# Optimization experiments

Hardware: AMD Instinct MI355X
Metric: run time of the kernel (lower is better)

Reference implementation:

```python
import jax, jax.numpy as jnp
import numpy as np

N = 50000      # nodes
E = 800000     # edges
D = 96         # in_dim = out_dim
ED = 17        # edge_dim = RBF_BINS + 1


def setup_inputs() -> dict:
    key = jax.random.key(0)
    ks = jax.random.split(key, 12)
    x = jax.random.normal(ks[0], (N, D), dtype=jnp.float32)
    edge_index = jax.random.randint(ks[1], (2, E), 0, N, dtype=jnp.int64)
    edge_attr = jax.random.uniform(ks[2], (E, ED), dtype=jnp.float32)
    s = 1.0 / np.sqrt(ED)
    W1 = jax.random.uniform(ks[3], (D, ED), jnp.float32, -s, s)
    b1 = jax.random.uniform(ks[4], (D,), jnp.float32, -s, s)
    s = 1.0 / np.sqrt(D)
    W2 = jax.random.uniform(ks[5], (D, D), jnp.float32, -s, s)
    b2 = jax.random.uniform(ks[6], (D,), jnp.float32, -s, s)
    Ws = jax.random.uniform(ks[7], (D, D), jnp.float32, -s, s)
    bs = jax.random.uniform(ks[8], (D,), jnp.float32, -s, s)
    Wn = jax.random.uniform(ks[9], (D, D), jnp.float32, -s, s)
    bn = jax.random.uniform(ks[10], (D,), jnp.float32, -s, s)
    return {"x": x, "edge_index": edge_index, "edge_attr": edge_attr,
            "W1": W1, "b1": b1, "W2": W2, "b2": b2,
            "Ws": Ws, "bs": bs, "Wn": Wn, "bn": bn}


def reference(x, edge_index, edge_attr, W1, b1, W2, b2, Ws, bs, Wn, bn):
    src, dst = edge_index[0], edge_index[1]
    # edge MLP: Linear -> ReLU -> Linear  => per-edge weight [E, D]
    h = jax.nn.relu(edge_attr @ W1.T + b1)
    w = h @ W2.T + b2
    # gather node features at src, weight, scatter-add into dst
    msg = w * x[src]                                   # [E, D]
    agg = jax.ops.segment_sum(msg, dst, num_segments=x.shape[0])  # [N, D]
    return jax.nn.relu(x @ Ws.T + bs + agg @ Wn.T + bn)
```

## Files before the change

kernel.cpp:

```cpp
#include <hip/hip_runtime.h>

#define BLOCK 512
#define TE 64
#define TN 64

typedef float f32x4 __attribute__((ext_vector_type(4)));
typedef short s16x8 __attribute__((ext_vector_type(8)));

static __device__ __forceinline__ unsigned short f2bf(float f) {
    unsigned int u = __float_as_uint(f);
    u += 0x7FFFu + ((u >> 16) & 1u);
    return (unsigned short)(u >> 16);
}
static __device__ __forceinline__ float bf2f(unsigned short s) {
    return __uint_as_float(((unsigned int)s) << 16);
}

__global__ __launch_bounds__(BLOCK, 4) void edge_kernel(
    const float* __restrict__ x,
    const int*   __restrict__ ei,
    const float* __restrict__ ea,
    const float* __restrict__ W1,
    const float* __restrict__ b1,
    const float* __restrict__ W2,
    const float* __restrict__ b2,
    float* __restrict__ agg,
    int N, int E)
{
    __shared__ unsigned short sW2h[96][104];
    __shared__ unsigned short sW2l[96][104];
    __shared__ unsigned short sh_hi[TE][104];
    __shared__ unsigned short sh_lo[TE][104];
    __shared__ float sW1[96][20];
    __shared__ float sea[TE][20];
    __shared__ float sb1[96];
    __shared__ int   ssrc[TE], sdst[TE];

    const int tid  = threadIdx.x;
    const int c    = tid & 31;
    const int g    = tid >> 5;
    const int lane = tid & 63;
    const int wv   = tid >> 6;
    const int mr   = wv & 3;
    const int ng   = wv >> 2;
    const int l15  = lane & 15;
    const int l4   = lane >> 4;

    for (int idx = tid; idx < 96 * 20; idx += BLOCK) {
        int d = idx / 20, k = idx - d * 20;
        sW1[d][k] = (k < 17) ? W1[d * 17 + k] : 0.f;
    }
    for (int idx = tid; idx < 96 * 96; idx += BLOCK) {
        int d = idx / 96, k = idx - d * 96;
        float v = W2[idx];
        unsigned short hb = f2bf(v);
        sW2h[d][k] = hb;
        sW2l[d][k] = f2bf(v - bf2f(hb));
    }
    if (tid < 96) sb1[tid] = b1[tid];

    float bias[3];
    #pragma unroll
    for (int t = 0; t < 3; ++t) bias[t] = b2[(ng * 3 + t) * 16 + l15];

    const int ntiles = (E + TE - 1) / TE;
    for (int tile = blockIdx.x; tile < ntiles; tile += gridDim.x) {
        const int e0 = tile * TE;
        __syncthreads();

        for (int idx = tid; idx < TE * 20; idx += BLOCK) {
            int e = idx / 20, k = idx - e * 20;
            float v = 0.f;
            if (k < 17 && e0 + e < E) v = ea[(size_t)(e0 + e) * 17 + k];
            sea[e][k] = v;
        }
        if (tid < TE) {
            int e = e0 + tid;
            ssrc[tid] = (e < E) ? ei[e] : 0;
            sdst[tid] = (e < E) ? ei[E + e] : 0;
        }
        __syncthreads();

        {
            float hacc[4][3];
            #pragma unroll
            for (int i = 0; i < 4; ++i) {
                hacc[i][0] = sb1[c]; hacc[i][1] = sb1[c + 32]; hacc[i][2] = sb1[c + 64];
            }
            #pragma unroll
            for (int k0 = 0; k0 < 20; k0 += 4) {
                float4 w0 = *(const float4*)&sW1[c][k0];
                float4 w1 = *(const float4*)&sW1[c + 32][k0];
                float4 w2 = *(const float4*)&sW1[c + 64][k0];
                #pragma unroll
                for (int i = 0; i < 4; ++i) {
                    float4 av = *(const float4*)&sea[g * 4 + i][k0];
                    hacc[i][0] = fmaf(av.w, w0.w, fmaf(av.z, w0.z, fmaf(av.y, w0.y, fmaf(av.x, w0.x, hacc[i][0]))));
                    hacc[i][1] = fmaf(av.w, w1.w, fmaf(av.z, w1.z, fmaf(av.y, w1.y, fmaf(av.x, w1.x, hacc[i][1]))));
                    hacc[i][2] = fmaf(av.w, w2.w, fmaf(av.z, w2.z, fmaf(av.y, w2.y, fmaf(av.x, w2.x, hacc[i][2]))));
                }
            }
            #pragma unroll
            for (int i = 0; i < 4; ++i) {
                int e = g * 4 + i;
                #pragma unroll
                for (int j = 0; j < 3; ++j) {
                    int d = c + 32 * j;
                    float v = fmaxf(hacc[i][j], 0.f);
                    unsigned short hb = f2bf(v);
                    sh_hi[e][d] = hb;
                    sh_lo[e][d] = f2bf(v - bf2f(hb));
                }
            }
        }
        __syncthreads();

        f32x4 acc[3];
        #pragma unroll
        for (int t = 0; t < 3; ++t) acc[t] = (f32x4){0.f, 0.f, 0.f, 0.f};

        const int arow = mr * 16 + l15;
        #pragma unroll
        for (int chunk = 0; chunk < 3; ++chunk) {
            const int koff = chunk * 32 + l4 * 8;
            s16x8 a_hi = *(const s16x8*)&sh_hi[arow][koff];
            s16x8 a_lo = *(const s16x8*)&sh_lo[arow][koff];
            #pragma unroll
            for (int t = 0; t < 3; ++t) {
                const int brow = (ng * 3 + t) * 16 + l15;
                s16x8 b_hi = *(const s16x8*)&sW2h[brow][koff];
                s16x8 b_lo = *(const s16x8*)&sW2l[brow][koff];
                acc[t] = __builtin_amdgcn_mfma_f32_16x16x32_bf16(a_hi, b_hi, acc[t], 0, 0, 0);
                acc[t] = __builtin_amdgcn_mfma_f32_16x16x32_bf16(a_hi, b_lo, acc[t], 0, 0, 0);
                acc[t] = __builtin_amdgcn_mfma_f32_16x16x32_bf16(a_lo, b_hi, acc[t], 0, 0, 0);
            }
        }

        #pragma unroll
        for (int t = 0; t < 3; ++t) {
            const int d = (ng * 3 + t) * 16 + l15;
            #pragma unroll
            for (int j = 0; j < 4; ++j) {
                const int el = mr * 16 + l4 * 4 + j;
                const int e  = e0 + el;
                if (e < E) {
                    float wval = acc[t][j] + bias[t];
                    int s = ssrc[el], dn = sdst[el];
                    atomicAdd(&agg[(size_t)dn * 96 + d], wval * x[(size_t)s * 96 + d]);
                }
            }
        }
    }
}

__global__ __launch_bounds__(BLOCK, 4) void node_kernel(
    const float* __restrict__ x,
    const float* __restrict__ agg,
    const float* __restrict__ Ws, const float* __restrict__ bs,
    const float* __restrict__ Wn, const float* __restrict__ bn,
    float* __restrict__ out, int N)
{
    __shared__ float sW[96][100];
    __shared__ float sxa[TN][100];
    __shared__ float sbias[96];

    const int tid = threadIdx.x;
    const int c = tid & 31, g = tid >> 5;
    const int n0 = blockIdx.x * TN;

    if (tid < 96) sbias[tid] = bs[tid] + bn[tid];

    float acc[4][3];
    #pragma unroll
    for (int i = 0; i < 4; ++i)
        for (int j = 0; j < 3; ++j) acc[i][j] = 0.f;

    for (int ph = 0; ph < 2; ++ph) {
        const float* __restrict__ W   = ph ? Wn : Ws;
        const float* __restrict__ src = ph ? agg : x;
        __syncthreads();
        for (int idx = tid; idx < 96 * 24; idx += BLOCK) {
            int d = idx / 24, kq = idx - d * 24;
            *(float4*)&sW[d][kq * 4] = *(const float4*)&W[d * 96 + kq * 4];
        }
        for (int idx = tid; idx < TN * 24; idx += BLOCK) {
            int n = idx / 24, kq = idx - n * 24;
            float4 v = make_float4(0.f, 0.f, 0.f, 0.f);
            if (n0 + n < N) v = *(const float4*)&src[(size_t)(n0 + n) * 96 + kq * 4];
            *(float4*)&sxa[n][kq * 4] = v;
        }
        __syncthreads();
        #pragma unroll 2
        for (int k0 = 0; k0 < 96; k0 += 4) {
            float4 w0 = *(const float4*)&sW[c][k0];
            float4 w1 = *(const float4*)&sW[c + 32][k0];
            float4 w2 = *(const float4*)&sW[c + 64][k0];
            #pragma unroll
            for (int i = 0; i < 4; ++i) {
                float4 xv = *(const float4*)&sxa[g * 4 + i][k0];
                acc[i][0] = fmaf(xv.w, w0.w, fmaf(xv.z, w0.z, fmaf(xv.y, w0.y, fmaf(xv.x, w0.x, acc[i][0]))));
                acc[i][1] = fmaf(xv.w, w1.w, fmaf(xv.z, w1.z, fmaf(xv.y, w1.y, fmaf(xv.x, w1.x, acc[i][1]))));
                acc[i][2] = fmaf(xv.w, w2.w, fmaf(xv.z, w2.z, fmaf(xv.y, w2.y, fmaf(xv.x, w2.x, acc[i][2]))));
            }
        }
    }

    #pragma unroll
    for (int i = 0; i < 4; ++i) {
        int n = n0 + g * 4 + i;
        if (n < N) {
            out[(size_t)n * 96 + c]      = fmaxf(acc[i][0] + sbias[c], 0.f);
            out[(size_t)n * 96 + c + 32] = fmaxf(acc[i][1] + sbias[c + 32], 0.f);
            out[(size_t)n * 96 + c + 64] = fmaxf(acc[i][2] + sbias[c + 64], 0.f);
        }
    }
}

extern "C" void kernel_launch(void* const* d_in, const int* in_sizes, int n_in,
                              void* d_out, int out_size, void* d_ws, size_t ws_size,
                              hipStream_t stream) {
    const float* x  = (const float*)d_in[0];
    const int*   ei = (const int*)d_in[1];
    const float* ea = (const float*)d_in[2];
    const float* W1 = (const float*)d_in[3];
    const float* b1 = (const float*)d_in[4];
    const float* W2 = (const float*)d_in[5];
    const float* b2 = (const float*)d_in[6];
    const float* Ws = (const float*)d_in[7];
    const float* bs = (const float*)d_in[8];
    const float* Wn = (const float*)d_in[9];
    const float* bn = (const float*)d_in[10];
    float* out = (float*)d_out;

    const int N = in_sizes[0] / 96;
    const int E = in_sizes[2] / 17;

    float* agg = (ws_size >= (size_t)N * 96 * sizeof(float)) ? (float*)d_ws : out;
    hipMemsetAsync(agg, 0, (size_t)N * 96 * sizeof(float), stream);

    edge_kernel<<<512, BLOCK, 0, stream>>>(x, ei, ea, W1, b1, W2, b2, agg, N, E);
    node_kernel<<<(N + TN - 1) / TN, BLOCK, 0, stream>>>(x, agg, Ws, bs, Wn, bn, out, N);
}
```

Measured before the change: 342.4 us.

## Software-pipeline edge tiles: prefetch next tile, defer atomics, pre-swizzle MFMA operands

Restructures the edge kernel loop so the next tile's edge attributes and indices are loaded into registers while the current tile computes. The x[src] gathers are issued before the MLP math, and the scatter atomics for the previous tile are deferred into the next iteration. W2 and the hidden activations are stored in LDS in an MFMA-fragment-ordered layout to make the operand loads contiguous and avoid bank conflicts. The goal is to hide global load and atomic latency, at the cost of more registers and possible occupancy loss.

```diff
diff --git a/kernel.cpp b/kernel.cpp
--- a/kernel.cpp
+++ b/kernel.cpp
@@ -3,6 +3,7 @@
 #define BLOCK 512
 #define TE 64
 #define TN 64
+#define NTB 512
 
 typedef float f32x4 __attribute__((ext_vector_type(4)));
 typedef short s16x8 __attribute__((ext_vector_type(8)));
@@ -27,10 +28,10 @@
     float* __restrict__ agg,
     int N, int E)
 {
-    __shared__ unsigned short sW2h[96][104];
-    __shared__ unsigned short sW2l[96][104];
-    __shared__ unsigned short sh_hi[TE][104];
-    __shared__ unsigned short sh_lo[TE][104];
+    __shared__ unsigned short sBh[9216];
+    __shared__ unsigned short sBl[9216];
+    __shared__ unsigned short sAh[3][TE][40];
+    __shared__ unsigned short sAl[3][TE][40];
     __shared__ float sW1[96][20];
     __shared__ float sea[TE][20];
     __shared__ float sb1[96];
@@ -46,6 +47,22 @@
     const int l15  = lane & 15;
     const int l4   = lane >> 4;
 
+    const int ntiles = (E + TE - 1) / TE;
+
+    const int pe = tid >> 3, ps = tid & 7;
+    float pf0 = 0.f, pf1 = 0.f, pf2 = 0.f; int pidx = 0;
+    int tile = blockIdx.x;
+    {
+        int e0n = tile * TE;
+        int ee  = e0n + pe; if (ee >= E) ee = E - 1;
+        const float* er = ea + (size_t)ee * 17;
+        pf0 = er[ps];
+        pf1 = er[ps + 8];
+        if (ps == 0) pf2 = er[16];
+        if (tid < TE)            { int e = e0n + tid;      pidx = (e < E) ? ei[e]     : 0; }
+        else if (tid < 2 * TE)   { int e = e0n + tid - TE; pidx = (e < E) ? ei[E + e] : 0; }
+    }
+
     for (int idx = tid; idx < 96 * 20; idx += BLOCK) {
         int d = idx / 20, k = idx - d * 20;
         sW1[d][k] = (k < 17) ? W1[d * 17 + k] : 0.f;
@@ -54,32 +71,72 @@
         int d = idx / 96, k = idx - d * 96;
         float v = W2[idx];
         unsigned short hb = f2bf(v);
-        sW2h[d][k] = hb;
-        sW2l[d][k] = f2bf(v - bf2f(hb));
+        int ngf = d / 48, tt = (d % 48) / 16, r = d & 15;
+        int ch = k >> 5, kl4 = (k & 31) >> 3, sb = k & 7;
+        int fo = ((((ngf * 3 + tt) * 3 + ch) * 4 + kl4) * 16 + r) * 8 + sb;
+        sBh[fo] = hb;
+        sBl[fo] = f2bf(v - bf2f(hb));
     }
     if (tid < 96) sb1[tid] = b1[tid];
-
-    float bias[3];
+    if (tid < TE) { sea[tid][17] = 0.f; sea[tid][18] = 0.f; sea[tid][19] = 0.f; }
+
+    float bias[3]; int dv[3];
     #pragma unroll
-    for (int t = 0; t < 3; ++t) bias[t] = b2[(ng * 3 + t) * 16 + l15];
-
-    const int ntiles = (E + TE - 1) / TE;
-    for (int tile = blockIdx.x; tile < ntiles; tile += gridDim.x) {
-        const int e0 = tile * TE;
-        __syncthreads();
-
-        for (int idx = tid; idx < TE * 20; idx += BLOCK) {
-            int e = idx / 20, k = idx - e * 20;
-            float v = 0.f;
-            if (k < 17 && e0 + e < E) v = ea[(size_t)(e0 + e) * 17 + k];
-            sea[e][k] = v;
-        }
-        if (tid < TE) {
-            int e = e0 + tid;
-            ssrc[tid] = (e < E) ? ei[e] : 0;
-            sdst[tid] = (e < E) ? ei[E + e] : 0;
-        }
-        __syncthreads();
+    for (int t = 0; t < 3; ++t) {
+        dv[t]   = (ng * 3 + t) * 16 + l15;
+        bias[t] = b2[dv[t]];
+    }
+
+    __syncthreads();
+
+    sea[pe][ps]     = pf0;
+    sea[pe][ps + 8] = pf1;
+    if (ps == 0) sea[pe][16] = pf2;
+    if (tid < TE)          ssrc[tid]      = pidx;
+    else if (tid < 2 * TE) sdst[tid - TE] = pidx;
+    __syncthreads();
+
+    float p_wvx[12]; int p_dn[4]; int p_e0 = 0;
+    const int first = blockIdx.x;
+
+    for (; tile < ntiles; tile += NTB) {
+        const int nxt = tile + NTB;
+
+        if (tile != first) {
+            #pragma unroll
+            for (int t = 0; t < 3; ++t)
+                #pragma unroll
+                for (int j = 0; j < 4; ++j) {
+                    int e = p_e0 + mr * 16 + l4 * 4 + j;
+                    if (e < E)
+                        atomicAdd(&agg[(size_t)p_dn[j] * 96 + dv[t]], p_wvx[t * 4 + j]);
+                }
+        }
+
+        if (nxt < ntiles) {
+            int e0n = nxt * TE;
+            int ee  = e0n + pe; if (ee >= E) ee = E - 1;
+            const float* er = ea + (size_t)ee * 17;
+            pf0 = er[ps];
+            pf1 = er[ps + 8];
+            if (ps == 0) pf2 = er[16];
+            if (tid < TE)            { int e = e0n + tid;      pidx = (e < E) ? ei[e]     : 0; }
+            else if (tid < 2 * TE)   { int e = e0n + tid - TE; pidx = (e < E) ? ei[E + e] : 0; }
+        }
+
+        int sg[4], ndn[4];
+        #pragma unroll
+        for (int j = 0; j < 4; ++j) {
+            int elj = mr * 16 + l4 * 4 + j;
+            sg[j]  = ssrc[elj];
+            ndn[j] = sdst[elj];
+        }
+        float xg[12];
+        #pragma unroll
+        for (int t = 0; t < 3; ++t)
+            #pragma unroll
+            for (int j = 0; j < 4; ++j)
+                xg[t * 4 + j] = x[(size_t)sg[j] * 96 + dv[t]];
 
         {
             float hacc[4][3];
@@ -105,11 +162,10 @@
                 int e = g * 4 + i;
                 #pragma unroll
                 for (int j = 0; j < 3; ++j) {
-                    int d = c + 32 * j;
                     float v = fmaxf(hacc[i][j], 0.f);
                     unsigned short hb = f2bf(v);
-                    sh_hi[e][d] = hb;
-                    sh_lo[e][d] = f2bf(v - bf2f(hb));
+                    sAh[j][e][c] = hb;
+                    sAl[j][e][c] = f2bf(v - bf2f(hb));
                 }
             }
         }
@@ -118,38 +174,51 @@
         f32x4 acc[3];
         #pragma unroll
         for (int t = 0; t < 3; ++t) acc[t] = (f32x4){0.f, 0.f, 0.f, 0.f};
-
         const int arow = mr * 16 + l15;
         #pragma unroll
         for (int chunk = 0; chunk < 3; ++chunk) {
-            const int koff = chunk * 32 + l4 * 8;
-            s16x8 a_hi = *(const s16x8*)&sh_hi[arow][koff];
-            s16x8 a_lo = *(const s16x8*)&sh_lo[arow][koff];
+            s16x8 a_hi = *(const s16x8*)&sAh[chunk][arow][l4 * 8];
+            s16x8 a_lo = *(const s16x8*)&sAl[chunk][arow][l4 * 8];
             #pragma unroll
             for (int t = 0; t < 3; ++t) {
-                const int brow = (ng * 3 + t) * 16 + l15;
-                s16x8 b_hi = *(const s16x8*)&sW2h[brow][koff];
-                s16x8 b_lo = *(const s16x8*)&sW2l[brow][koff];
+                const int base = (((ng * 3 + t) * 3 + chunk) * 64 + lane) * 8;
+                s16x8 b_hi = *(const s16x8*)&sBh[base];
+                s16x8 b_lo = *(const s16x8*)&sBl[base];
                 acc[t] = __builtin_amdgcn_mfma_f32_16x16x32_bf16(a_hi, b_hi, acc[t], 0, 0, 0);
                 acc[t] = __builtin_amdgcn_mfma_f32_16x16x32_bf16(a_hi, b_lo, acc[t], 0, 0, 0);
                 acc[t] = __builtin_amdgcn_mfma_f32_16x16x32_bf16(a_lo, b_hi, acc[t], 0, 0, 0);
             }
         }
 
-        #pragma unroll
-        for (int t = 0; t < 3; ++t) {
-            const int d = (ng * 3 + t) * 16 + l15;
+        if (nxt < ntiles) {
+            sea[pe][ps]     = pf0;
+            sea[pe][ps + 8] = pf1;
+            if (ps == 0) sea[pe][16] = pf2;
+            if (tid < TE)          ssrc[tid]      = pidx;
+            else if (tid < 2 * TE) sdst[tid - TE] = pidx;
+        }
+
+        #pragma unroll
+        for (int t = 0; t < 3; ++t)
+            #pragma unroll
+            for (int j = 0; j < 4; ++j)
+                p_wvx[t * 4 + j] = (acc[t][j] + bias[t]) * xg[t * 4 + j];
+        #pragma unroll
+        for (int j = 0; j < 4; ++j) p_dn[j] = ndn[j];
+        p_e0 = tile * TE;
+
+        __syncthreads();
+    }
+
+    if (first < ntiles) {
+        #pragma unroll
+        for (int t = 0; t < 3; ++t)
             #pragma unroll
             for (int j = 0; j < 4; ++j) {
-                const int el = mr * 16 + l4 * 4 + j;
-                const int e  = e0 + el;
-                if (e < E) {
-                    float wval = acc[t][j] + bias[t];
-                    int s = ssrc[el], dn = sdst[el];
-                    atomicAdd(&agg[(size_t)dn * 96 + d], wval * x[(size_t)s * 96 + d]);
-                }
-            }
-        }
+                int e = p_e0 + mr * 16 + l4 * 4 + j;
+                if (e < E)
+                    atomicAdd(&agg[(size_t)p_dn[j] * 96 + dv[t]], p_wvx[t * 4 + j]);
+            }
     }
 }
 
@@ -238,6 +307,6 @@
     float* agg = (ws_size >= (size_t)N * 96 * sizeof(float)) ? (float*)d_ws : out;
     hipMemsetAsync(agg, 0, (size_t)N * 96 * sizeof(float), stream);
 
-    edge_kernel<<<512, BLOCK, 0, stream>>>(x, ei, ea, W1, b1, W2, b2, agg, N, E);
+    edge_kernel<<<NTB, BLOCK, 0, stream>>>(x, ei, ea, W1, b1, W2, b2, agg, N, E);
     node_kernel<<<(N + TN - 1) / TN, BLOCK, 0, stream>>>(x, agg, Ws, bs, Wn, bn, out, N);
 }
```

After: 319.4 us. 1.07x faster.
